# Performance work log

Hardware: AMD Instinct MI355X
Metric: run time of the kernel (lower is better)

## Reference

```python
import jax, jax.numpy as jnp
import numpy as np

B, D, K, H, E, Z = 64, 25000, 16, 128, 256, 32


def setup_inputs() -> dict:
    key = jax.random.key(0)
    ks = jax.random.split(key, 10)
    s = 0.02
    return {
        "x": jax.random.normal(ks[0], (B, D), jnp.float32),
        "mask": jax.random.randint(ks[1], (B, D), 0, 2, jnp.int32),
        "feat_emb": jax.random.normal(ks[2], (D, K), jnp.float32),          # feature_embedding [D,K]
        "feat_bias": jnp.zeros((D, 1), jnp.float32),                        # feature_bias [D,1]
        "W1": jax.random.normal(ks[3], (1 + K + 1, H), jnp.float32) * s,    # h_layer linear 1 (in,out)
        "b1": jnp.zeros((H,), jnp.float32),
        "W2": jax.random.normal(ks[4], (H, K), jnp.float32) * s,            # h_layer linear 2
        "b2": jnp.zeros((K,), jnp.float32),
        "We1": jax.random.normal(ks[5], (K, E), jnp.float32) * s,           # encoder_mlp linear 1
        "be1": jnp.zeros((E,), jnp.float32),
        "We2": jax.random.normal(ks[6], (E, 2 * Z), jnp.float32) * s,       # encoder_mlp linear 2
        "be2": jnp.zeros((2 * Z,), jnp.float32),
    }


def reference(x, mask, feat_emb, feat_bias, W1, b1, W2, b2, We1, be1, We2, be2):
    b, d = x.shape
    k = feat_emb.shape[1]
    # Build per-(sample, feature) input rows: [x_bd, F_d(K), bias_d] -> [B, D, 1+K+1]
    h_in = jnp.concatenate(
        [
            x[:, :, None],
            jnp.broadcast_to(feat_emb[None, :, :], (b, d, k)),
            jnp.broadcast_to(feat_bias[None, :, :], (b, d, 1)),
        ],
        axis=-1,
    )
    # Shared small MLP (h_layer), dropout is identity at rate 0.0
    h = jax.nn.relu(h_in @ W1 + b1)          # [B, D, H]
    h = jax.nn.relu(h @ W2 + b2)             # [B, D, K]
    # Masked sum pooling over features
    c = jnp.sum(h * mask.astype(h.dtype)[:, :, None], axis=1)  # [B, K]
    # encoder_mlp
    enc = jax.nn.relu(c @ We1 + be1) @ We2 + be2                # [B, 2Z]
    mu, logvar = jnp.split(enc, 2, axis=-1)
    return mu, logvar
```

## Files before the change

kernel.cpp:

```cpp
#include <hip/hip_runtime.h>

#define B 64
#define D 25000
#define K 16
#define H 128
#define E 256
#define Z 32
#define DTILE 16
#define NT_TILES 1563
#define TILES_PER_BLK 2
#define NPB 782
#define NREP 8
#define XSTR 68

#define REP_BYTES (NREP * B * K * 4)

typedef __attribute__((ext_vector_type(8))) _Float16 half8;
typedef __attribute__((ext_vector_type(4))) _Float16 hv4;
typedef __attribute__((ext_vector_type(2))) _Float16 hv2;
typedef __attribute__((ext_vector_type(4))) float f32x4;

__global__ __launch_bounds__(256) void main_kernel(
    const float* __restrict__ x, const int* __restrict__ mask,
    const float* __restrict__ feat_emb, const float* __restrict__ feat_bias,
    const float* __restrict__ W1, const float* __restrict__ b1,
    const float* __restrict__ W2, const float* __restrict__ b2,
    float* __restrict__ rep)
{
    __shared__ __align__(16) _Float16 sGh[2][DTILE * H];
    __shared__ __align__(16) _Float16 sXh[2][DTILE * XSTR];
    __shared__ __align__(16) _Float16 sMh[2][DTILE * XSTR];

    const int t    = threadIdx.x;
    const int lane = t & 63;
    const int wv   = t >> 6;
    const int g    = lane >> 4;
    const int n    = lane & 15;

    half8 Bf[4];
    #pragma unroll
    for (int s = 0; s < 4; ++s) {
        union { half8 v; _Float16 e[8]; } u;
        #pragma unroll
        for (int j = 0; j < 8; ++j)
            u.e[j] = (_Float16)W2[(s * 32 + g * 8 + j) * K + n];
        Bf[s] = u.v;
    }
    hv2 w0h[4][4];
    #pragma unroll
    for (int s = 0; s < 4; ++s) {
        const float4* wp = (const float4*)&W1[s * 32 + g * 8];
        float4 a0 = wp[0], a1 = wp[1];
        w0h[s][0] = (hv2){(_Float16)a0.x, (_Float16)a0.y};
        w0h[s][1] = (hv2){(_Float16)a0.z, (_Float16)a0.w};
        w0h[s][2] = (hv2){(_Float16)a1.x, (_Float16)a1.y};
        w0h[s][3] = (hv2){(_Float16)a1.z, (_Float16)a1.w};
    }
    half8 bfG[2];
    #pragma unroll
    for (int cc = 0; cc < 2; ++cc) {
        const int h = (wv * 2 + cc) * 16 + n;
        union { half8 v; _Float16 e[8]; } u;
        #pragma unroll
        for (int j = 0; j < 8; ++j) {
            const int k = g * 8 + j;
            float v;
            if (k < 16)       v = W1[(1 + k) * H + h];
            else if (k == 16) v = W1[17 * H + h];
            else if (k == 17) v = b1[h];
            else              v = 0.f;
            u.e[j] = (_Float16)v;
        }
        bfG[cc] = u.v;
    }
    const float b2n = b2[n];
    const hv2 zeroh = {(_Float16)0.f, (_Float16)0.f};
    const int moff = wv * 16 + g * 4;
    const int sample = wv * 16 + n;

    const int t0 = blockIdx.x * TILES_PER_BLK;
    const int t1 = min(t0 + TILES_PER_BLK, NT_TILES);

    auto STAGE = [&](int buf, int tile) {
        const int bb = t >> 2;
        const int dd = (t & 3) * 4;
        const int dg = tile * DTILE + dd;
        float xv[4], mv[4];
        if (dg + 4 <= D) {
            float4 xx = *(const float4*)&x[(size_t)bb * D + dg];
            int4   mm = *(const int4*)&mask[(size_t)bb * D + dg];
            xv[0] = xx.x; xv[1] = xx.y; xv[2] = xx.z; xv[3] = xx.w;
            mv[0] = (float)mm.x; mv[1] = (float)mm.y; mv[2] = (float)mm.z; mv[3] = (float)mm.w;
        } else {
            #pragma unroll
            for (int i = 0; i < 4; ++i) {
                const int dgi = dg + i;
                xv[i] = (dgi < D) ? x[(size_t)bb * D + dgi] : 0.f;
                mv[i] = (dgi < D) ? (float)mask[(size_t)bb * D + dgi] : 0.f;
            }
        }
        #pragma unroll
        for (int i = 0; i < 4; ++i) {
            sXh[buf][(dd + i) * XSTR + bb] = (_Float16)xv[i];
            sMh[buf][(dd + i) * XSTR + bb] = (_Float16)mv[i];
        }
    };

    auto GCOMP = [&](int buf, int tile) {
        const int dA = min(tile * DTILE + n, D - 1);
        union { half8 v; _Float16 e[8]; } af;
        if (g < 2) {
            const float4* fe = (const float4*)&feat_emb[(size_t)dA * K + g * 8];
            float4 u0 = fe[0], u1 = fe[1];
            af.e[0] = (_Float16)u0.x; af.e[1] = (_Float16)u0.y;
            af.e[2] = (_Float16)u0.z; af.e[3] = (_Float16)u0.w;
            af.e[4] = (_Float16)u1.x; af.e[5] = (_Float16)u1.y;
            af.e[6] = (_Float16)u1.z; af.e[7] = (_Float16)u1.w;
        } else if (g == 2) {
            af.e[0] = (_Float16)feat_bias[dA];
            af.e[1] = (_Float16)1.f;
            #pragma unroll
            for (int j = 2; j < 8; ++j) af.e[j] = (_Float16)0.f;
        } else {
            #pragma unroll
            for (int j = 0; j < 8; ++j) af.e[j] = (_Float16)0.f;
        }
        #pragma unroll
        for (int cc = 0; cc < 2; ++cc) {
            f32x4 C = {0.f, 0.f, 0.f, 0.f};
            C = __builtin_amdgcn_mfma_f32_16x16x32_f16(af.v, bfG[cc], C, 0, 0, 0);
            #pragma unroll
            for (int r = 0; r < 4; ++r)
                sGh[buf][(g * 4 + r) * H + (wv * 2 + cc) * 16 + n] = (_Float16)C[r];
        }
    };

    f32x4 cacc = {0.f, 0.f, 0.f, 0.f};

    STAGE(0, t0);
    GCOMP(0, t0);
    __syncthreads();

    int cur = 0;
    for (int tt = t0; tt < t1; ++tt) {
        if (tt + 1 < t1) { STAGE(cur ^ 1, tt + 1); GCOMP(cur ^ 1, tt + 1); }

        hv2 xh[DTILE / 2];
        #pragma unroll
        for (int i = 0; i < DTILE / 2; ++i)
            xh[i] = (hv2){sXh[cur][(2 * i) * XSTR + sample],
                          sXh[cur][(2 * i + 1) * XSTR + sample]};
        const _Float16* gb0 = sGh[cur] + g * 8;

        #pragma unroll
        for (int i = 0; i < DTILE / 2; ++i) {
            const int dd0 = 2 * i, dd1 = 2 * i + 1;
            const hv2 xa = {xh[i].x, xh[i].x};
            const hv2 xb = {xh[i].y, xh[i].y};
            f32x4 c1a = {b2n, b2n, b2n, b2n};
            f32x4 c1b = {b2n, b2n, b2n, b2n};
            #pragma unroll
            for (int s = 0; s < 4; ++s) {
                union GA { half8 v; hv2 p[4]; };
                GA ga, gb, A0, A1;
                ga.v = *(const half8*)(gb0 + dd0 * H + s * 32);
                gb.v = *(const half8*)(gb0 + dd1 * H + s * 32);
                #pragma unroll
                for (int p = 0; p < 4; ++p) {
                    hv2 h0 = __builtin_elementwise_fma(xa, w0h[s][p], ga.p[p]);
                    hv2 h1 = __builtin_elementwise_fma(xb, w0h[s][p], gb.p[p]);
                    A0.p[p] = __builtin_elementwise_max(h0, zeroh);
                    A1.p[p] = __builtin_elementwise_max(h1, zeroh);
                }
                c1a = __builtin_amdgcn_mfma_f32_16x16x32_f16(A0.v, Bf[s], c1a, 0, 0, 0);
                c1b = __builtin_amdgcn_mfma_f32_16x16x32_f16(A1.v, Bf[s], c1b, 0, 0, 0);
            }
            hv4 m0 = *(const hv4*)&sMh[cur][dd0 * XSTR + moff];
            hv4 m1 = *(const hv4*)&sMh[cur][dd1 * XSTR + moff];
            cacc[0] = fmaf((float)m0.x, fmaxf(c1a[0], 0.f), fmaf((float)m1.x, fmaxf(c1b[0], 0.f), cacc[0]));
            cacc[1] = fmaf((float)m0.y, fmaxf(c1a[1], 0.f), fmaf((float)m1.y, fmaxf(c1b[1], 0.f), cacc[1]));
            cacc[2] = fmaf((float)m0.z, fmaxf(c1a[2], 0.f), fmaf((float)m1.z, fmaxf(c1b[2], 0.f), cacc[2]));
            cacc[3] = fmaf((float)m0.w, fmaxf(c1a[3], 0.f), fmaf((float)m1.w, fmaxf(c1b[3], 0.f), cacc[3]));
        }
        __syncthreads();
        cur ^= 1;
    }

    float* crep = rep + (size_t)(blockIdx.x & (NREP - 1)) * (B * K);
    #pragma unroll
    for (int r = 0; r < 4; ++r)
        atomicAdd(&crep[(moff + r) * K + n], cacc[r]);
}

__global__ __launch_bounds__(256) void partial_enc_kernel(
    const float* __restrict__ rep, const float* __restrict__ We1,
    const float* __restrict__ be1, const float* __restrict__ We2,
    const float* __restrict__ be2, float* __restrict__ out)
{
    const int b = blockIdx.x;
    const int t = threadIdx.x;
    __shared__ float sc[K];
    __shared__ float st1[E];
    __shared__ float red[256];

    {
        const int k = t & 15, grp = t >> 4;
        red[t] = (grp < NREP) ? rep[grp * (B * K) + b * K + k] : 0.f;
    }
    __syncthreads();
    if (t < K) {
        float s2 = 0.f;
        #pragma unroll
        for (int q = 0; q < 16; ++q) s2 += red[q * 16 + t];
        sc[t] = s2;
    }
    __syncthreads();

    {
        float acc = be1[t];
        #pragma unroll
        for (int k = 0; k < K; ++k)
            acc = fmaf(sc[k], We1[k * E + t], acc);
        st1[t] = fmaxf(acc, 0.f);
    }
    __syncthreads();

    const int j = t & 63, seg = t >> 6;
    float acc = 0.f;
    #pragma unroll 4
    for (int e = seg * 64; e < seg * 64 + 64; ++e)
        acc = fmaf(st1[e], We2[e * 64 + j], acc);
    red[t] = acc;
    __syncthreads();

    if (t < 64) {
        float v = red[j] + red[64 + j] + red[128 + j] + red[192 + j] + be2[j];
        if (j < Z) out[b * Z + j] = v;
        else       out[B * Z + b * Z + (j - Z)] = v;
    }
}

extern "C" void kernel_launch(void* const* d_in, const int* in_sizes, int n_in,
                              void* d_out, int out_size, void* d_ws, size_t ws_size,
                              hipStream_t stream) {
    const float* x         = (const float*)d_in[0];
    const int*   mask      = (const int*)  d_in[1];
    const float* feat_emb  = (const float*)d_in[2];
    const float* feat_bias = (const float*)d_in[3];
    const float* W1        = (const float*)d_in[4];
    const float* b1        = (const float*)d_in[5];
    const float* W2        = (const float*)d_in[6];
    const float* b2        = (const float*)d_in[7];
    const float* We1       = (const float*)d_in[8];
    const float* be1       = (const float*)d_in[9];
    const float* We2       = (const float*)d_in[10];
    const float* be2       = (const float*)d_in[11];

    float* rep = (float*)d_ws;

    hipMemsetAsync(rep, 0, REP_BYTES, stream);
    main_kernel<<<NPB, 256, 0, stream>>>(
        x, mask, feat_emb, feat_bias, W1, b1, W2, b2, rep);
    partial_enc_kernel<<<B, 256, 0, stream>>>(
        rep, We1, be1, We2, be2, (float*)d_out);
}
```

Measured before the change: 115.6 us.

## Use persistent grid-stride tiles with per-block partials instead of atomics

The main kernel now launches 512 blocks that stride over all D-tiles instead of 782 blocks with two tiles each. Each block writes its own partial sums to a slot, which removes the global atomics and the memset, and the encoder kernel reduces all 512 partials per sample. The mask is staged in LDS as float rather than half, which avoids conversions but doubles that buffer, and launch bounds request two blocks per CU. The trade is fewer, longer-lived blocks with more double-buffer reuse, against a larger final reduction (512×B×K floats) in the small encoder kernel.

New measurement: 112.1 us. 1.03x faster.

```diff
diff --git a/kernel.cpp b/kernel.cpp
--- a/kernel.cpp
+++ b/kernel.cpp
@@ -7,29 +7,25 @@
 #define E 256
 #define Z 32
 #define DTILE 16
-#define NT_TILES 1563
-#define TILES_PER_BLK 2
-#define NPB 782
-#define NREP 8
+#define NT_TILES ((D + DTILE - 1) / DTILE)
+#define NPB 512
 #define XSTR 68
-
-#define REP_BYTES (NREP * B * K * 4)
+#define MSTR 68
 
 typedef __attribute__((ext_vector_type(8))) _Float16 half8;
-typedef __attribute__((ext_vector_type(4))) _Float16 hv4;
 typedef __attribute__((ext_vector_type(2))) _Float16 hv2;
 typedef __attribute__((ext_vector_type(4))) float f32x4;
 
-__global__ __launch_bounds__(256) void main_kernel(
+__global__ __launch_bounds__(256, 2) void main_kernel(
     const float* __restrict__ x, const int* __restrict__ mask,
     const float* __restrict__ feat_emb, const float* __restrict__ feat_bias,
     const float* __restrict__ W1, const float* __restrict__ b1,
     const float* __restrict__ W2, const float* __restrict__ b2,
-    float* __restrict__ rep)
+    float* __restrict__ part)
 {
     __shared__ __align__(16) _Float16 sGh[2][DTILE * H];
     __shared__ __align__(16) _Float16 sXh[2][DTILE * XSTR];
-    __shared__ __align__(16) _Float16 sMh[2][DTILE * XSTR];
+    __shared__ __align__(16) float    sMf[2][DTILE * MSTR];
 
     const int t    = threadIdx.x;
     const int lane = t & 63;
@@ -77,9 +73,6 @@
     const hv2 zeroh = {(_Float16)0.f, (_Float16)0.f};
     const int moff = wv * 16 + g * 4;
     const int sample = wv * 16 + n;
-
-    const int t0 = blockIdx.x * TILES_PER_BLK;
-    const int t1 = min(t0 + TILES_PER_BLK, NT_TILES);
 
     auto STAGE = [&](int buf, int tile) {
         const int bb = t >> 2;
@@ -102,7 +95,7 @@
         #pragma unroll
         for (int i = 0; i < 4; ++i) {
             sXh[buf][(dd + i) * XSTR + bb] = (_Float16)xv[i];
-            sMh[buf][(dd + i) * XSTR + bb] = (_Float16)mv[i];
+            sMf[buf][(dd + i) * MSTR + bb] = mv[i];
         }
     };
 
@@ -137,13 +130,15 @@
 
     f32x4 cacc = {0.f, 0.f, 0.f, 0.f};
 
-    STAGE(0, t0);
-    GCOMP(0, t0);
+    int tt = blockIdx.x;
+    STAGE(0, tt);
+    GCOMP(0, tt);
     __syncthreads();
 
     int cur = 0;
-    for (int tt = t0; tt < t1; ++tt) {
-        if (tt + 1 < t1) { STAGE(cur ^ 1, tt + 1); GCOMP(cur ^ 1, tt + 1); }
+    for (; tt < NT_TILES; tt += NPB) {
+        const int nxt = tt + NPB;
+        if (nxt < NT_TILES) { STAGE(cur ^ 1, nxt); GCOMP(cur ^ 1, nxt); }
 
         hv2 xh[DTILE / 2];
         #pragma unroll
@@ -175,25 +170,25 @@
                 c1a = __builtin_amdgcn_mfma_f32_16x16x32_f16(A0.v, Bf[s], c1a, 0, 0, 0);
                 c1b = __builtin_amdgcn_mfma_f32_16x16x32_f16(A1.v, Bf[s], c1b, 0, 0, 0);
             }
-            hv4 m0 = *(const hv4*)&sMh[cur][dd0 * XSTR + moff];
-            hv4 m1 = *(const hv4*)&sMh[cur][dd1 * XSTR + moff];
-            cacc[0] = fmaf((float)m0.x, fmaxf(c1a[0], 0.f), fmaf((float)m1.x, fmaxf(c1b[0], 0.f), cacc[0]));
-            cacc[1] = fmaf((float)m0.y, fmaxf(c1a[1], 0.f), fmaf((float)m1.y, fmaxf(c1b[1], 0.f), cacc[1]));
-            cacc[2] = fmaf((float)m0.z, fmaxf(c1a[2], 0.f), fmaf((float)m1.z, fmaxf(c1b[2], 0.f), cacc[2]));
-            cacc[3] = fmaf((float)m0.w, fmaxf(c1a[3], 0.f), fmaf((float)m1.w, fmaxf(c1b[3], 0.f), cacc[3]));
+            float4 m0 = *(const float4*)&sMf[cur][dd0 * MSTR + moff];
+            float4 m1 = *(const float4*)&sMf[cur][dd1 * MSTR + moff];
+            cacc[0] = fmaf(m0.x, fmaxf(c1a[0], 0.f), fmaf(m1.x, fmaxf(c1b[0], 0.f), cacc[0]));
+            cacc[1] = fmaf(m0.y, fmaxf(c1a[1], 0.f), fmaf(m1.y, fmaxf(c1b[1], 0.f), cacc[1]));
+            cacc[2] = fmaf(m0.z, fmaxf(c1a[2], 0.f), fmaf(m1.z, fmaxf(c1b[2], 0.f), cacc[2]));
+            cacc[3] = fmaf(m0.w, fmaxf(c1a[3], 0.f), fmaf(m1.w, fmaxf(c1b[3], 0.f), cacc[3]));
         }
         __syncthreads();
         cur ^= 1;
     }
 
-    float* crep = rep + (size_t)(blockIdx.x & (NREP - 1)) * (B * K);
+    float* crep = part + (size_t)blockIdx.x * (B * K);
     #pragma unroll
     for (int r = 0; r < 4; ++r)
-        atomicAdd(&crep[(moff + r) * K + n], cacc[r]);
+        crep[(moff + r) * K + n] = cacc[r];
 }
 
 __global__ __launch_bounds__(256) void partial_enc_kernel(
-    const float* __restrict__ rep, const float* __restrict__ We1,
+    const float* __restrict__ part, const float* __restrict__ We1,
     const float* __restrict__ be1, const float* __restrict__ We2,
     const float* __restrict__ be2, float* __restrict__ out)
 {
@@ -204,8 +199,12 @@
     __shared__ float red[256];
 
     {
-        const int k = t & 15, grp = t >> 4;
-        red[t] = (grp < NREP) ? rep[grp * (B * K) + b * K + k] : 0.f;
+        const int k = t & 15;
+        float acc0 = 0.f;
+        #pragma unroll 4
+        for (int p = t >> 4; p < NPB; p += 16)
+            acc0 += part[(size_t)p * (B * K) + b * K + k];
+        red[t] = acc0;
     }
     __syncthreads();
     if (t < K) {
@@ -256,11 +255,10 @@
     const float* We2       = (const float*)d_in[10];
     const float* be2       = (const float*)d_in[11];
 
-    float* rep = (float*)d_ws;
-
-    hipMemsetAsync(rep, 0, REP_BYTES, stream);
+    float* part = (float*)d_ws;
+
     main_kernel<<<NPB, 256, 0, stream>>>(
-        x, mask, feat_emb, feat_bias, W1, b1, W2, b2, rep);
+        x, mask, feat_emb, feat_bias, W1, b1, W2, b2, part);
     partial_enc_kernel<<<B, 256, 0, stream>>>(
-        rep, We1, be1, We2, be2, (float*)d_out);
+        part, We1, be1, We2, be2, (float*)d_out);
 }
```
